# Kernel tuning notes

Measured on AMD Instinct MI355X. Metric: run time of the kernel, lower is better.

## Reference

```python
import jax, jax.numpy as jnp
import numpy as np

EMB_DIM = 128
HEAD_SIZE = 16  # embDim // numHea = 128 // 8


def setup_inputs() -> dict:
    key = jax.random.key(0)
    k1, k2, k3, k4 = jax.random.split(key, 4)
    B, T = 8, 2048
    inpEmb = jax.random.normal(k1, (B, T, EMB_DIM), dtype=jnp.float32)
    # nn.Linear(embDim, heaSiz, bias=False) weights, stored transposed so y = x @ W
    Wq = jax.random.normal(k2, (EMB_DIM, HEAD_SIZE), dtype=jnp.float32) / np.sqrt(EMB_DIM)
    Wk = jax.random.normal(k3, (EMB_DIM, HEAD_SIZE), dtype=jnp.float32) / np.sqrt(EMB_DIM)
    Wv = jax.random.normal(k4, (EMB_DIM, HEAD_SIZE), dtype=jnp.float32) / np.sqrt(EMB_DIM)
    return {"inpEmb": inpEmb, "Wq": Wq, "Wk": Wk, "Wv": Wv}


def reference(inpEmb, Wq, Wk, Wv):
    # q,k,v: [B, T, H]
    q = inpEmb @ Wq
    k = inpEmb @ Wk
    v = inpEmb @ Wv
    scale = HEAD_SIZE ** -0.5
    # scores: [B, T, T]
    scores = jnp.einsum('bqh,bkh->bqk', q, k) * scale
    T = inpEmb.shape[1]
    causal = jnp.tril(jnp.ones((T, T), dtype=bool))
    scores = jnp.where(causal, scores, -jnp.inf)
    weights = jax.nn.softmax(scores, axis=-1)
    # dropout treated as identity (eval mode) for deterministic reference
    return jnp.einsum('bqk,bkh->bqh', weights, v)
```

## Files before the change

### kernel.cpp

```cpp
#include <hip/hip_runtime.h>
#include <hip/hip_bf16.h>

#define T_SEQ 2048
#define EMB   128
#define H     16
#define BATCH 8
#define BQ    64
#define QSCALE 0.360673760222241f

#define EXP2F(x) __builtin_amdgcn_exp2f(x)

typedef short short8_t __attribute__((ext_vector_type(8)));
typedef float f32x4    __attribute__((ext_vector_type(4)));

__device__ __forceinline__ unsigned short f2bf(float f) {
    __hip_bfloat16 h = __float2bfloat16(f);
    return *reinterpret_cast<unsigned short*>(&h);
}

__global__ __launch_bounds__(256) void qkv_kernel(
    const float* __restrict__ x,
    const float* __restrict__ Wq,
    const float* __restrict__ Wk,
    const float* __restrict__ Wv,
    unsigned short* __restrict__ Qbf,
    unsigned short* __restrict__ Kbf,
    unsigned short* __restrict__ Vt)
{
    __shared__ unsigned short Wt[3][16][136];

    const int tid = threadIdx.x;
#pragma unroll
    for (int p = 0; p < 6; ++p) {
        const int idx4 = tid + p * 256;
        const int flat = idx4 * 4;
        const int mm   = flat >> 11;
        const int rem  = flat & 2047;
        const int d    = rem >> 4;
        const int c0   = rem & 15;
        const float* Wm = (mm == 0) ? Wq : (mm == 1) ? Wk : Wv;
        float4 w = *reinterpret_cast<const float4*>(Wm + rem);
        Wt[mm][c0    ][d] = f2bf(w.x);
        Wt[mm][c0 + 1][d] = f2bf(w.y);
        Wt[mm][c0 + 2][d] = f2bf(w.z);
        Wt[mm][c0 + 3][d] = f2bf(w.w);
    }
    __syncthreads();

    const int w4   = tid >> 6;
    const int lane = tid & 63;
    const int q    = lane >> 4;
    const int n    = lane & 15;
    const int row0 = blockIdx.x * 64 + w4 * 16;
    const float* xr = x + (size_t)(row0 + n) * EMB;

    f32x4 aq = {0,0,0,0}, ak = {0,0,0,0}, av = {0,0,0,0};
#pragma unroll
    for (int t = 0; t < 4; ++t) {
        const int k0 = t * 32 + q * 8;
        float4 xa = *reinterpret_cast<const float4*>(xr + k0);
        float4 xb = *reinterpret_cast<const float4*>(xr + k0 + 4);
        union { unsigned short s[8]; short8_t v; } xf;
        xf.s[0]=f2bf(xa.x); xf.s[1]=f2bf(xa.y); xf.s[2]=f2bf(xa.z); xf.s[3]=f2bf(xa.w);
        xf.s[4]=f2bf(xb.x); xf.s[5]=f2bf(xb.y); xf.s[6]=f2bf(xb.z); xf.s[7]=f2bf(xb.w);
        short8_t wqf = *reinterpret_cast<const short8_t*>(&Wt[0][n][k0]);
        short8_t wkf = *reinterpret_cast<const short8_t*>(&Wt[1][n][k0]);
        short8_t wvf = *reinterpret_cast<const short8_t*>(&Wt[2][n][k0]);
        aq = __builtin_amdgcn_mfma_f32_16x16x32_bf16(xf.v, wqf, aq, 0, 0, 0);
        ak = __builtin_amdgcn_mfma_f32_16x16x32_bf16(xf.v, wkf, ak, 0, 0, 0);
        av = __builtin_amdgcn_mfma_f32_16x16x32_bf16(xf.v, wvf, av, 0, 0, 0);
    }

    const int grow = row0 + q * 4;
    const int b    = grow >> 11;
    const int ib0  = grow & 2047;
#pragma unroll
    for (int r = 0; r < 4; ++r) {
        Qbf[(size_t)(grow + r) * H + n] = f2bf(aq[r] * QSCALE);
        Kbf[(size_t)(grow + r) * H + n] = f2bf(ak[r]);
    }
    union { unsigned short s[4]; unsigned long long u; } vp;
    vp.s[0]=f2bf(av[0]); vp.s[1]=f2bf(av[1]); vp.s[2]=f2bf(av[2]); vp.s[3]=f2bf(av[3]);
    *reinterpret_cast<unsigned long long*>(
        Vt + ((size_t)b * H + n) * T_SEQ + ib0) = vp.u;
}

__global__ __launch_bounds__(256) void attn_phase1(
    const unsigned short* __restrict__ Qbf,
    const unsigned short* __restrict__ Kbf,
    const unsigned short* __restrict__ Vt,
    float* __restrict__ P2, int cs, int maxp)
{
    __shared__ unsigned int Pbuf[4][32][17];

    const int qt   = blockIdx.x;
    const int cch  = blockIdx.y;
    const int b    = blockIdx.z;
    const int i0   = qt * BQ;
    const int kbeg = cch << cs;
    if (kbeg >= i0 + BQ) return;

    const int tid  = threadIdx.x;
    const int w    = tid >> 6;
    const int lane = tid & 63;
    const int q    = lane >> 4;
    const int n    = lane & 15;
    const int wrow0 = i0 + w * 16;
    const int irow  = wrow0 + n;
    const int kend  = min(kbeg + (1 << cs), wrow0 + 16);
    const int ntiles = (kend - kbeg + 63) >> 6;

    const unsigned short* Qp = Qbf + (size_t)b * T_SEQ * H;
    const unsigned short* Kp = Kbf + (size_t)b * T_SEQ * H;
    const unsigned short* Vp = Vt  + (size_t)b * H * T_SEQ;

    short8_t qf = {0,0,0,0,0,0,0,0};
    if (q < 2)
        qf = *reinterpret_cast<const short8_t*>(Qp + (size_t)irow * H + q * 8);

    f32x4 acc = {0.f, 0.f, 0.f, 0.f};
    float m = -1e30f, l = 0.f;

    for (int kt = 0; kt < ntiles; ++kt) {
        const int j0 = kbeg + kt * 64;

        f32x4 S[4];
#pragma unroll
        for (int s = 0; s < 4; ++s) {
            short8_t kf = {0,0,0,0,0,0,0,0};
            if (q < 2)
                kf = *reinterpret_cast<const short8_t*>(
                        Kp + (size_t)(j0 + s * 16 + n) * H + q * 8);
            f32x4 z = {0.f, 0.f, 0.f, 0.f};
            S[s] = __builtin_amdgcn_mfma_f32_16x16x32_bf16(kf, qf, z, 0, 0, 0);
        }

        short8_t vf0 = *reinterpret_cast<const short8_t*>(
                Vp + (size_t)n * T_SEQ + (j0 + q * 8));
        short8_t vf1 = *reinterpret_cast<const short8_t*>(
                Vp + (size_t)n * T_SEQ + (j0 + 32 + q * 8));

        float tm = -1e30f;
        if (j0 + 63 > wrow0) {
#pragma unroll
            for (int s = 0; s < 4; ++s) {
                const int kb = j0 + s * 16 + q * 4;
#pragma unroll
                for (int r = 0; r < 4; ++r) {
                    float v = (kb + r <= irow) ? S[s][r] : -1e30f;
                    S[s][r] = v;
                    tm = fmaxf(tm, v);
                }
            }
        } else {
#pragma unroll
            for (int s = 0; s < 4; ++s) {
                tm = fmaxf(tm, fmaxf(fmaxf(S[s][0], S[s][1]),
                                     fmaxf(S[s][2], S[s][3])));
            }
        }
        tm = fmaxf(tm, __shfl_xor(tm, 16));
        tm = fmaxf(tm, __shfl_xor(tm, 32));
        const float mn    = fmaxf(m, tm);
        const float alpha = EXP2F(m - mn);
        m = mn;

        float ps = 0.f;
#pragma unroll
        for (int s = 0; s < 4; ++s) {
            float e0 = EXP2F(S[s][0] - mn);
            float e1 = EXP2F(S[s][1] - mn);
            float e2 = EXP2F(S[s][2] - mn);
            float e3 = EXP2F(S[s][3] - mn);
            ps += (e0 + e1) + (e2 + e3);
            unsigned int b0 = __builtin_bit_cast(unsigned int, e0);
            unsigned int b1 = __builtin_bit_cast(unsigned int, e1);
            unsigned int b2 = __builtin_bit_cast(unsigned int, e2);
            unsigned int b3 = __builtin_bit_cast(unsigned int, e3);
            Pbuf[w][s * 8 + q * 2 + 0][n] = (b1 & 0xffff0000u) | (b0 >> 16);
            Pbuf[w][s * 8 + q * 2 + 1][n] = (b3 & 0xffff0000u) | (b2 >> 16);
        }
        ps += __shfl_xor(ps, 16);
        ps += __shfl_xor(ps, 32);
        l = l * alpha + ps;
        acc[0] *= alpha; acc[1] *= alpha; acc[2] *= alpha; acc[3] *= alpha;

        {
            union { unsigned int u[4]; short8_t v; } pu;
            pu.u[0] = Pbuf[w][q * 4 + 0][n];
            pu.u[1] = Pbuf[w][q * 4 + 1][n];
            pu.u[2] = Pbuf[w][q * 4 + 2][n];
            pu.u[3] = Pbuf[w][q * 4 + 3][n];
            acc = __builtin_amdgcn_mfma_f32_16x16x32_bf16(vf0, pu.v, acc, 0, 0, 0);
            pu.u[0] = Pbuf[w][16 + q * 4 + 0][n];
            pu.u[1] = Pbuf[w][16 + q * 4 + 1][n];
            pu.u[2] = Pbuf[w][16 + q * 4 + 2][n];
            pu.u[3] = Pbuf[w][16 + q * 4 + 3][n];
            acc = __builtin_amdgcn_mfma_f32_16x16x32_bf16(vf1, pu.v, acc, 0, 0, 0);
        }
    }

    float* pp = P2 + ((size_t)(b * T_SEQ + irow) * maxp + cch) * 18;
    float2 r01; r01.x = acc[0]; r01.y = acc[1];
    float2 r23; r23.x = acc[2]; r23.y = acc[3];
    *reinterpret_cast<float2*>(pp + q * 4)     = r01;
    *reinterpret_cast<float2*>(pp + q * 4 + 2) = r23;
    if (q == 0) { pp[16] = m; pp[17] = l; }
}

__global__ __launch_bounds__(256) void attn_phase2(
    const float* __restrict__ P2, float* __restrict__ out, int cs, int maxp)
{
    const int gid = blockIdx.x * 256 + threadIdx.x;
    const int row = gid >> 4;
    const int d   = gid & 15;
    const int ib  = row & (T_SEQ - 1);
    const int nc  = (ib >> cs) + 1;
    const float* base = P2 + (size_t)row * maxp * 18;

    float M = -1e30f;
    for (int p = 0; p < nc; ++p) M = fmaxf(M, base[p * 18 + 16]);
    float L = 0.f, o = 0.f;
    for (int p = 0; p < nc; ++p) {
        const float wgt = EXP2F(base[p * 18 + 16] - M);
        L += wgt * base[p * 18 + 17];
        o += wgt * base[p * 18 + d];
    }
    out[gid] = o / L;
}

extern "C" void kernel_launch(void* const* d_in, const int* in_sizes, int n_in,
                              void* d_out, int out_size, void* d_ws, size_t ws_size,
                              hipStream_t stream)
{
    const float* x  = (const float*)d_in[0];
    const float* Wq = (const float*)d_in[1];
    const float* Wk = (const float*)d_in[2];
    const float* Wv = (const float*)d_in[3];
    float* out = (float*)d_out;

    const size_t NE = (size_t)BATCH * T_SEQ * H;
    unsigned short* Qbf = (unsigned short*)d_ws;
    unsigned short* Kbf = Qbf + NE;
    unsigned short* Vt  = Kbf + NE;
    float* P2 = (float*)(Vt + NE);

    const size_t need8 = 3 * NE * 2 + (size_t)BATCH * T_SEQ * 8 * 18 * 4;
    int cs, maxp;
    if (ws_size >= need8) { cs = 8; maxp = 8; }
    else                  { cs = 9; maxp = 4; }

    qkv_kernel<<<BATCH * T_SEQ / 64, 256, 0, stream>>>(x, Wq, Wk, Wv, Qbf, Kbf, Vt);
    attn_phase1<<<dim3(T_SEQ / BQ, maxp, BATCH), 256, 0, stream>>>(
        Qbf, Kbf, Vt, P2, cs, maxp);
    attn_phase2<<<(int)(NE / 256), 256, 0, stream>>>(P2, out, cs, maxp);
}
```

Measured before the change: 89.79 us.

## Fuse split-K combine into attention kernel via atomic last-block reduction

Merges the partial-attention and combine kernels. The last block to finish a query tile, detected with an atomic counter that qkv_kernel zeroes, performs the log-sum-exp merge, which removes one kernel launch. It also enumerates only the causally non-empty (query tile, chunk) pairs, heaviest first, so no blocks are launched just to exit early. Each iteration now covers 128 keys with vectorized LDS writes and reads of P, and the row-sum shuffle reduction moves out of the loop. The costs are more registers and reliance on threadfence/atomic ordering, and the chunk size is hardwired to 256 with no smaller-workspace fallback.

```diff
diff --git a/kernel.cpp b/kernel.cpp
--- a/kernel.cpp
+++ b/kernel.cpp
@@ -6,6 +6,7 @@
 #define H     16
 #define BATCH 8
 #define BQ    64
+#define MAXP  8
 #define QSCALE 0.360673760222241f
 
 #define EXP2F(x) __builtin_amdgcn_exp2f(x)
@@ -25,11 +26,14 @@
     const float* __restrict__ Wv,
     unsigned short* __restrict__ Qbf,
     unsigned short* __restrict__ Kbf,
-    unsigned short* __restrict__ Vt)
+    unsigned short* __restrict__ Vt,
+    int* __restrict__ cnt)
 {
     __shared__ unsigned short Wt[3][16][136];
 
     const int tid = threadIdx.x;
+    if (blockIdx.x == 0) cnt[tid] = 0;
+
 #pragma unroll
     for (int p = 0; p < 6; ++p) {
         const int idx4 = tid + p * 256;
@@ -47,11 +51,11 @@
     }
     __syncthreads();
 
-    const int w4   = tid >> 6;
+    const int wv   = tid >> 6;
     const int lane = tid & 63;
     const int q    = lane >> 4;
     const int n    = lane & 15;
-    const int row0 = blockIdx.x * 64 + w4 * 16;
+    const int row0 = blockIdx.x * 64 + wv * 16;
     const float* xr = x + (size_t)(row0 + n) * EMB;
 
     f32x4 aq = {0,0,0,0}, ak = {0,0,0,0}, av = {0,0,0,0};
@@ -85,34 +89,43 @@
         Vt + ((size_t)b * H + n) * T_SEQ + ib0) = vp.u;
 }
 
-__global__ __launch_bounds__(256) void attn_phase1(
+__global__ __launch_bounds__(256) void attn_fused(
     const unsigned short* __restrict__ Qbf,
     const unsigned short* __restrict__ Kbf,
     const unsigned short* __restrict__ Vt,
-    float* __restrict__ P2, int cs, int maxp)
+    float* __restrict__ P2,
+    int* __restrict__ cnt,
+    float* __restrict__ out)
 {
-    __shared__ unsigned int Pbuf[4][32][17];
-
-    const int qt   = blockIdx.x;
-    const int cch  = blockIdx.y;
-    const int b    = blockIdx.z;
-    const int i0   = qt * BQ;
-    const int kbeg = cch << cs;
-    if (kbeg >= i0 + BQ) return;
+    __shared__ unsigned int Pbuf[4][16][136];
+    __shared__ int sCombine;
+
+    const int b = blockIdx.y;
+    const int r = 143 - blockIdx.x;
+    int g = 0;
+    while (r >= 2 * (g + 1) * (g + 2)) ++g;
+    const int idx = r - 2 * g * (g + 1);
+    const int qq  = idx / (g + 1);
+    const int qt  = 4 * g + qq;
+    const int cch = idx - qq * (g + 1);
+    const int nc  = g + 1;
+
+    const int i0   = qt << 6;
+    const int kbeg = cch << 8;
 
     const int tid  = threadIdx.x;
-    const int w    = tid >> 6;
+    const int wv   = tid >> 6;
     const int lane = tid & 63;
     const int q    = lane >> 4;
     const int n    = lane & 15;
-    const int wrow0 = i0 + w * 16;
+    const int wrow0 = i0 + wv * 16;
     const int irow  = wrow0 + n;
-    const int kend  = min(kbeg + (1 << cs), wrow0 + 16);
-    const int ntiles = (kend - kbeg + 63) >> 6;
+    const int kend  = min(kbeg + 256, wrow0 + 16);
+    const int nit   = (kend - kbeg + 127) >> 7;
 
     const unsigned short* Qp = Qbf + (size_t)b * T_SEQ * H;
     const unsigned short* Kp = Kbf + (size_t)b * T_SEQ * H;
-    const unsigned short* Vp = Vt  + (size_t)b * H * T_SEQ;
+    const unsigned short* vrow = Vt + (size_t)b * H * T_SEQ + (size_t)n * T_SEQ;
 
     short8_t qf = {0,0,0,0,0,0,0,0};
     if (q < 2)
@@ -121,12 +134,13 @@
     f32x4 acc = {0.f, 0.f, 0.f, 0.f};
     float m = -1e30f, l = 0.f;
 
-    for (int kt = 0; kt < ntiles; ++kt) {
-        const int j0 = kbeg + kt * 64;
-
-        f32x4 S[4];
-#pragma unroll
-        for (int s = 0; s < 4; ++s) {
+    for (int it = 0; it < nit; ++it) {
+        const int j0   = kbeg + (it << 7);
+        const int base = (it & 1) << 6;
+
+        f32x4 S[8];
+#pragma unroll
+        for (int s = 0; s < 8; ++s) {
             short8_t kf = {0,0,0,0,0,0,0,0};
             if (q < 2)
                 kf = *reinterpret_cast<const short8_t*>(
@@ -134,30 +148,28 @@
             f32x4 z = {0.f, 0.f, 0.f, 0.f};
             S[s] = __builtin_amdgcn_mfma_f32_16x16x32_bf16(kf, qf, z, 0, 0, 0);
         }
-
-        short8_t vf0 = *reinterpret_cast<const short8_t*>(
-                Vp + (size_t)n * T_SEQ + (j0 + q * 8));
-        short8_t vf1 = *reinterpret_cast<const short8_t*>(
-                Vp + (size_t)n * T_SEQ + (j0 + 32 + q * 8));
+        short8_t vf[4];
+#pragma unroll
+        for (int h = 0; h < 4; ++h)
+            vf[h] = *reinterpret_cast<const short8_t*>(vrow + j0 + h * 32 + q * 8);
 
         float tm = -1e30f;
-        if (j0 + 63 > wrow0) {
-#pragma unroll
-            for (int s = 0; s < 4; ++s) {
+        if (j0 + 127 > wrow0) {
+#pragma unroll
+            for (int s = 0; s < 8; ++s) {
                 const int kb = j0 + s * 16 + q * 4;
 #pragma unroll
-                for (int r = 0; r < 4; ++r) {
-                    float v = (kb + r <= irow) ? S[s][r] : -1e30f;
-                    S[s][r] = v;
+                for (int rr = 0; rr < 4; ++rr) {
+                    float v = (kb + rr <= irow) ? S[s][rr] : -1e30f;
+                    S[s][rr] = v;
                     tm = fmaxf(tm, v);
                 }
             }
         } else {
 #pragma unroll
-            for (int s = 0; s < 4; ++s) {
+            for (int s = 0; s < 8; ++s)
                 tm = fmaxf(tm, fmaxf(fmaxf(S[s][0], S[s][1]),
                                      fmaxf(S[s][2], S[s][3])));
-            }
         }
         tm = fmaxf(tm, __shfl_xor(tm, 16));
         tm = fmaxf(tm, __shfl_xor(tm, 32));
@@ -167,7 +179,7 @@
 
         float ps = 0.f;
 #pragma unroll
-        for (int s = 0; s < 4; ++s) {
+        for (int s = 0; s < 8; ++s) {
             float e0 = EXP2F(S[s][0] - mn);
             float e1 = EXP2F(S[s][1] - mn);
             float e2 = EXP2F(S[s][2] - mn);
@@ -177,56 +189,60 @@
             unsigned int b1 = __builtin_bit_cast(unsigned int, e1);
             unsigned int b2 = __builtin_bit_cast(unsigned int, e2);
             unsigned int b3 = __builtin_bit_cast(unsigned int, e3);
-            Pbuf[w][s * 8 + q * 2 + 0][n] = (b1 & 0xffff0000u) | (b0 >> 16);
-            Pbuf[w][s * 8 + q * 2 + 1][n] = (b3 & 0xffff0000u) | (b2 >> 16);
-        }
-        ps += __shfl_xor(ps, 16);
-        ps += __shfl_xor(ps, 32);
+            unsigned long long pw =
+                (unsigned long long)((b1 & 0xffff0000u) | (b0 >> 16)) |
+                ((unsigned long long)((b3 & 0xffff0000u) | (b2 >> 16)) << 32);
+            *reinterpret_cast<unsigned long long*>(
+                &Pbuf[wv][n][base + 8 * s + 2 * q]) = pw;
+        }
         l = l * alpha + ps;
         acc[0] *= alpha; acc[1] *= alpha; acc[2] *= alpha; acc[3] *= alpha;
 
-        {
-            union { unsigned int u[4]; short8_t v; } pu;
-            pu.u[0] = Pbuf[w][q * 4 + 0][n];
-            pu.u[1] = Pbuf[w][q * 4 + 1][n];
-            pu.u[2] = Pbuf[w][q * 4 + 2][n];
-            pu.u[3] = Pbuf[w][q * 4 + 3][n];
-            acc = __builtin_amdgcn_mfma_f32_16x16x32_bf16(vf0, pu.v, acc, 0, 0, 0);
-            pu.u[0] = Pbuf[w][16 + q * 4 + 0][n];
-            pu.u[1] = Pbuf[w][16 + q * 4 + 1][n];
-            pu.u[2] = Pbuf[w][16 + q * 4 + 2][n];
-            pu.u[3] = Pbuf[w][16 + q * 4 + 3][n];
-            acc = __builtin_amdgcn_mfma_f32_16x16x32_bf16(vf1, pu.v, acc, 0, 0, 0);
-        }
-    }
-
-    float* pp = P2 + ((size_t)(b * T_SEQ + irow) * maxp + cch) * 18;
+#pragma unroll
+        for (int h = 0; h < 4; ++h) {
+            uint4 p4 = *reinterpret_cast<const uint4*>(
+                    &Pbuf[wv][n][base + 16 * h + 4 * q]);
+            union { uint4 u; short8_t v; } pu; pu.u = p4;
+            acc = __builtin_amdgcn_mfma_f32_16x16x32_bf16(vf[h], pu.v, acc, 0, 0, 0);
+        }
+    }
+
+    l += __shfl_xor(l, 16);
+    l += __shfl_xor(l, 32);
+
+    float* pp = P2 + ((size_t)(b * T_SEQ + irow) * MAXP + cch) * 18;
     float2 r01; r01.x = acc[0]; r01.y = acc[1];
     float2 r23; r23.x = acc[2]; r23.y = acc[3];
     *reinterpret_cast<float2*>(pp + q * 4)     = r01;
     *reinterpret_cast<float2*>(pp + q * 4 + 2) = r23;
     if (q == 0) { pp[16] = m; pp[17] = l; }
-}
-
-__global__ __launch_bounds__(256) void attn_phase2(
-    const float* __restrict__ P2, float* __restrict__ out, int cs, int maxp)
-{
-    const int gid = blockIdx.x * 256 + threadIdx.x;
-    const int row = gid >> 4;
-    const int d   = gid & 15;
-    const int ib  = row & (T_SEQ - 1);
-    const int nc  = (ib >> cs) + 1;
-    const float* base = P2 + (size_t)row * maxp * 18;
-
-    float M = -1e30f;
-    for (int p = 0; p < nc; ++p) M = fmaxf(M, base[p * 18 + 16]);
-    float L = 0.f, o = 0.f;
-    for (int p = 0; p < nc; ++p) {
-        const float wgt = EXP2F(base[p * 18 + 16] - M);
-        L += wgt * base[p * 18 + 17];
-        o += wgt * base[p * 18 + d];
-    }
-    out[gid] = o / L;
+
+    __threadfence();
+    __syncthreads();
+    if (tid == 0) {
+        int old = atomicAdd(&cnt[b * 32 + qt], 1);
+        sCombine = (old == nc - 1);
+    }
+    __syncthreads();
+    if (!sCombine) return;
+    __threadfence();
+
+#pragma unroll
+    for (int rr = 0; rr < 4; ++rr) {
+        const int gidx = tid + rr * 256;
+        const int row  = gidx >> 4;
+        const int d    = gidx & 15;
+        const float* basep = P2 + (size_t)(b * T_SEQ + i0 + row) * (MAXP * 18);
+        float M = -1e30f;
+        for (int p = 0; p < nc; ++p) M = fmaxf(M, basep[p * 18 + 16]);
+        float L = 0.f, o = 0.f;
+        for (int p = 0; p < nc; ++p) {
+            const float wgt = EXP2F(basep[p * 18 + 16] - M);
+            L += wgt * basep[p * 18 + 17];
+            o += wgt * basep[p * 18 + d];
+        }
+        out[(size_t)(b * T_SEQ + i0 + row) * H + d] = o / L;
+    }
 }
 
 extern "C" void kernel_launch(void* const* d_in, const int* in_sizes, int n_in,
@@ -244,14 +260,10 @@
     unsigned short* Kbf = Qbf + NE;
     unsigned short* Vt  = Kbf + NE;
     float* P2 = (float*)(Vt + NE);
-
-    const size_t need8 = 3 * NE * 2 + (size_t)BATCH * T_SEQ * 8 * 18 * 4;
-    int cs, maxp;
-    if (ws_size >= need8) { cs = 8; maxp = 8; }
-    else                  { cs = 9; maxp = 4; }
-
-    qkv_kernel<<<BATCH * T_SEQ / 64, 256, 0, stream>>>(x, Wq, Wk, Wv, Qbf, Kbf, Vt);
-    attn_phase1<<<dim3(T_SEQ / BQ, maxp, BATCH), 256, 0, stream>>>(
-        Qbf, Kbf, Vt, P2, cs, maxp);
-    attn_phase2<<<(int)(NE / 256), 256, 0, stream>>>(P2, out, cs, maxp);
-}
+    int*   cnt = (int*)(P2 + (size_t)BATCH * T_SEQ * MAXP * 18);
+
+    qkv_kernel<<<BATCH * T_SEQ / 64, 256, 0, stream>>>(
+        x, Wq, Wk, Wv, Qbf, Kbf, Vt, cnt);
+    attn_fused<<<dim3(144, BATCH), 256, 0, stream>>>(
+        Qbf, Kbf, Vt, P2, cnt, out);
+}
```

Result: slower. 278.3 us (+209.9%).
